# Optimization experiments

Measured on AMD Instinct MI355X. Metric: run time of the kernel, lower is better.

Reference implementation:

```python
import jax, jax.numpy as jnp
import numpy as np

N, DIN, C, E = 50000, 256, 8, 1600000
N_STEPS = 5


def setup_inputs() -> dict:
    key = jax.random.key(0)
    k1, k2, k3, k4 = jax.random.split(key, 4)
    x = jax.random.normal(k1, (N, DIN), dtype=jnp.float32)
    W = jax.random.normal(k2, (DIN, C), dtype=jnp.float32) / np.float32(np.sqrt(DIN))
    b = jnp.zeros((C,), dtype=jnp.float32)
    edge_index = jax.random.randint(k3, (2, E), 0, N, dtype=jnp.int64)
    rv = jax.random.randint(k4, (E,), 0, E, dtype=jnp.int64)
    return {"x": x, "W": W, "b": b, "edge_index": edge_index, "rv": rv}


def _log_normalize(lx):
    return lx - jax.scipy.special.logsumexp(lx, axis=-1, keepdims=True)


def reference(x, W, b, edge_index, rv):
    # transform: Linear (num_hidden=0) + LogSoftmax -> initial log beliefs
    log_b0 = jax.nn.log_softmax(x @ W + b, axis=-1)            # [N, C]
    src, dst = edge_index[0], edge_index[1]
    n_nodes, n_cls = log_b0.shape
    # learn_coupling=False: log_H = -3 * (ones - eye)
    logH = -3.0 * (jnp.ones((n_cls, n_cls), jnp.float32) - jnp.eye(n_cls, dtype=jnp.float32))
    log_msg = jnp.full((edge_index.shape[1], n_cls), -np.log(n_cls), dtype=jnp.float32)
    log_b = log_b0
    for _ in range(N_STEPS):
        x_j = log_b[src]                                        # [E, C] gather
        t = x_j - log_msg[rv]                                   # [E, C]
        # per-edge logsumexp over incoming class dim against coupling matrix
        raw = jax.scipy.special.logsumexp(t[:, :, None] + logH[None, :, :], axis=1)  # [E, C]
        log_msg = _log_normalize(raw)
        agg = jax.ops.segment_sum(log_msg, dst, num_segments=n_nodes)  # scatter-add
        log_b = _log_normalize(agg + log_b0)
    return log_b
```

## Files before the change

kernel.cpp:

```cpp
#include <hip/hip_runtime.h>

static constexpr int kN   = 50000;
static constexpr int kDin = 256;
static constexpr int kC   = 8;
static constexpr int kE   = 1600000;
static constexpr int kSteps = 5;

static constexpr int kNB        = 256;
static constexpr int kBucketW   = 196;
static constexpr int kChunk     = 4096;

static constexpr size_t OFF_LOGB0 = 0;
static constexpr size_t OFF_BHIST = 1600000;
static constexpr size_t OFF_GBASE = 1601024;
static constexpr size_t OFF_GCUR  = 1602112;
static constexpr size_t OFF_START = 1603200;
static constexpr size_t OFF_REC   = 1803264;
static constexpr size_t OFF_INV   = 8203264;
static constexpr size_t OFF_MSGA  = 14603264;
static constexpr size_t OFF_MSGB  = 40203264;
static constexpr size_t WS_NEEDED = 65803264;

static constexpr float kDEC   = 3.0f / 65535.0f;
static constexpr float kENC   = 65535.0f / 3.0f;
static constexpr float kOFF   = 3.2990003f;
static constexpr float kA     = 0.049787068367863944f;
static constexpr float kOneMA = 0.950212931632136f;

__global__ void __launch_bounds__(256) init_kernel(
    const float* __restrict__ x, const float* __restrict__ W,
    const float* __restrict__ bias,
    float* __restrict__ log_b0, float* __restrict__ log_b,
    const int* __restrict__ dst, int* __restrict__ bhist)
{
    __shared__ int h[kNB];
    if (blockIdx.x >= 1024) {
        h[threadIdx.x] = 0;
        __syncthreads();
        const int nthr = 256 * 256;
        for (int e = (blockIdx.x - 1024) * 256 + threadIdx.x; e < kE; e += nthr)
            atomicAdd(&h[dst[e] / kBucketW], 1);
        __syncthreads();
        if (h[threadIdx.x]) atomicAdd(&bhist[threadIdx.x], h[threadIdx.x]);
        return;
    }

    const int lane   = threadIdx.x & 63;
    const int wave   = (blockIdx.x * 256 + threadIdx.x) >> 6;
    const int nwaves = (1024 * 256) >> 6;

    float w[4][8];
#pragma unroll
    for (int j = 0; j < 4; ++j) {
        const float4* wp = reinterpret_cast<const float4*>(W + (size_t)(lane + 64 * j) * kC);
        float4 a = wp[0], b2 = wp[1];
        w[j][0] = a.x;  w[j][1] = a.y;  w[j][2] = a.z;  w[j][3] = a.w;
        w[j][4] = b2.x; w[j][5] = b2.y; w[j][6] = b2.z; w[j][7] = b2.w;
    }

    for (int row = wave; row < kN; row += nwaves) {
        const float* xr = x + (size_t)row * kDin;
        float acc[8] = {0.f, 0.f, 0.f, 0.f, 0.f, 0.f, 0.f, 0.f};
#pragma unroll
        for (int j = 0; j < 4; ++j) {
            float xv = xr[lane + 64 * j];
#pragma unroll
            for (int c = 0; c < 8; ++c) acc[c] = fmaf(xv, w[j][c], acc[c]);
        }
#pragma unroll
        for (int off = 32; off > 0; off >>= 1) {
#pragma unroll
            for (int c = 0; c < 8; ++c) acc[c] += __shfl_down(acc[c], off, 64);
        }
        if (lane == 0) {
            float z[8], m = -1e30f;
#pragma unroll
            for (int c = 0; c < 8; ++c) { z[c] = acc[c] + bias[c]; m = fmaxf(m, z[c]); }
            float s = 0.f;
#pragma unroll
            for (int c = 0; c < 8; ++c) s += __expf(z[c] - m);
            float lse = m + __logf(s);
#pragma unroll
            for (int c = 0; c < 8; ++c) {
                float v = z[c] - lse;
                log_b0[(size_t)row * 8 + c] = v;
                log_b[(size_t)row * 8 + c]  = v;
            }
        }
    }
}

__global__ void __launch_bounds__(256) bucket_scan_kernel(
    const int* __restrict__ bhist, int* __restrict__ gbase, int* __restrict__ gcur)
{
    __shared__ int sh[kNB];
    const int tid = threadIdx.x;
    int v = bhist[tid];
    sh[tid] = v;
    __syncthreads();
#pragma unroll
    for (int off = 1; off < kNB; off <<= 1) {
        int t = (tid >= off) ? sh[tid - off] : 0;
        __syncthreads();
        sh[tid] += t;
        __syncthreads();
    }
    int excl = sh[tid] - v;
    gbase[tid] = excl;
    gcur[tid]  = excl;
    if (tid == kNB - 1) { gbase[kNB] = sh[tid]; gcur[kNB] = sh[tid]; }
}

__global__ void __launch_bounds__(256) bin_kernel(
    const int* __restrict__ dst, int* __restrict__ gcur,
    unsigned int* __restrict__ recbuf)
{
    __shared__ int hist[kNB];
    __shared__ int sh[kNB];
    __shared__ int cursor[kNB];
    __shared__ int gdbase[kNB];
    __shared__ unsigned int buf[kChunk];

    const int tid = threadIdx.x;
    const int e0  = blockIdx.x * kChunk;
    const int n   = (kE - e0 < kChunk) ? (kE - e0) : kChunk;

    hist[tid] = 0;
    __syncthreads();

    int myb[16];
    unsigned int rec[16];
#pragma unroll
    for (int k = 0; k < 16; ++k) {
        const int i = tid + k * 256;
        myb[k] = -1;
        if (i < n) {
            const int d = dst[e0 + i];
            const int b = d / kBucketW;
            myb[k] = b;
            rec[k] = ((unsigned int)(d - b * kBucketW) << 21) | (unsigned int)(e0 + i);
            atomicAdd(&hist[b], 1);
        }
    }
    __syncthreads();

    const int cnt = hist[tid];
    sh[tid] = cnt;
    __syncthreads();
#pragma unroll
    for (int off = 1; off < kNB; off <<= 1) {
        int t = (tid >= off) ? sh[tid - off] : 0;
        __syncthreads();
        sh[tid] += t;
        __syncthreads();
    }
    const int excl = sh[tid] - cnt;
    cursor[tid] = excl;
    __syncthreads();

#pragma unroll
    for (int k = 0; k < 16; ++k) {
        if (myb[k] >= 0) {
            int slot = atomicAdd(&cursor[myb[k]], 1);
            buf[slot] = rec[k];
        }
    }
    gdbase[tid] = (cnt > 0) ? atomicAdd(&gcur[tid], cnt) : 0;
    __syncthreads();

    for (int i = tid; i < n; i += 256) {
        int b = 0;
#pragma unroll
        for (int step = 128; step >= 1; step >>= 1)
            if (b + step <= kNB - 1 && sh[b + step - 1] <= i) b += step;
        const int off_in_b = i - (sh[b] - hist[b]);
        recbuf[gdbase[b] + off_in_b] = buf[i];
    }
}

__global__ void __launch_bounds__(256) fine_kernel(
    const int* __restrict__ gbase, const unsigned int* __restrict__ recbuf,
    int* __restrict__ start, int* __restrict__ inv)
{
    __shared__ int hist[kNB];
    __shared__ int sh[kNB];
    __shared__ int lcur[kNB];

    const int tid = threadIdx.x;
    const int b   = blockIdx.x;
    const int nb0 = b * kBucketW;
    const int nnode = (kN - nb0 < kBucketW) ? (kN - nb0) : kBucketW;
    const int rb = gbase[b], re = gbase[b + 1];

    hist[tid] = 0;
    __syncthreads();

    for (int i = rb + tid; i < re; i += 256)
        atomicAdd(&hist[recbuf[i] >> 21], 1);
    __syncthreads();

    const int cnt = hist[tid];
    sh[tid] = cnt;
    __syncthreads();
#pragma unroll
    for (int off = 1; off < kNB; off <<= 1) {
        int t = (tid >= off) ? sh[tid - off] : 0;
        __syncthreads();
        sh[tid] += t;
        __syncthreads();
    }
    const int excl = sh[tid] - cnt;
    lcur[tid] = rb + excl;
    if (tid < nnode) start[nb0 + tid] = rb + excl;
    if (b == gridDim.x - 1 && tid == 0) start[kN] = kE;
    __syncthreads();

    for (int i = rb + tid; i < re; i += 256) {
        const unsigned int r = recbuf[i];
        const int p = atomicAdd(&lcur[r >> 21], 1);
        inv[p] = (int)(r & 0x1FFFFFu);
    }
}

template <bool FIRST>
__global__ void __launch_bounds__(256) edge_kernel(
    const int* __restrict__ src, const int* __restrict__ rv,
    const float* __restrict__ log_b,
    const unsigned short* __restrict__ mold,
    unsigned short* __restrict__ mnew)
{
    const int e0 = (blockIdx.x * 256 + threadIdx.x) * 2;
    if (e0 >= kE) return;

    const int2 sp = *reinterpret_cast<const int2*>(src + e0);

    const float4* lba = reinterpret_cast<const float4*>(log_b + (size_t)sp.x * 8);
    const float4* lbb = reinterpret_cast<const float4*>(log_b + (size_t)sp.y * 8);
    float4 a0 = lba[0], a1 = lba[1];
    float4 b0 = lbb[0], b1 = lbb[1];

    uint4 ma, mb;
    if (!FIRST) {
        const int2 rp = *reinterpret_cast<const int2*>(rv + e0);
        ma = *reinterpret_cast<const uint4*>(mold + (size_t)rp.x * 8);
        mb = *reinterpret_cast<const uint4*>(mold + (size_t)rp.y * 8);
    }

    float ta[8] = {a0.x, a0.y, a0.z, a0.w, a1.x, a1.y, a1.z, a1.w};
    float tb[8] = {b0.x, b0.y, b0.z, b0.w, b1.x, b1.y, b1.z, b1.w};
    if (!FIRST) {
        ta[0] -= (float)(ma.x & 0xffffu) * kDEC;  ta[1] -= (float)(ma.x >> 16) * kDEC;
        ta[2] -= (float)(ma.y & 0xffffu) * kDEC;  ta[3] -= (float)(ma.y >> 16) * kDEC;
        ta[4] -= (float)(ma.z & 0xffffu) * kDEC;  ta[5] -= (float)(ma.z >> 16) * kDEC;
        ta[6] -= (float)(ma.w & 0xffffu) * kDEC;  ta[7] -= (float)(ma.w >> 16) * kDEC;
        tb[0] -= (float)(mb.x & 0xffffu) * kDEC;  tb[1] -= (float)(mb.x >> 16) * kDEC;
        tb[2] -= (float)(mb.y & 0xffffu) * kDEC;  tb[3] -= (float)(mb.y >> 16) * kDEC;
        tb[4] -= (float)(mb.z & 0xffffu) * kDEC;  tb[5] -= (float)(mb.z >> 16) * kDEC;
        tb[6] -= (float)(mb.w & 0xffffu) * kDEC;  tb[7] -= (float)(mb.w >> 16) * kDEC;
    }

    unsigned int qa[8], qb[8];
    {
        float mx = ta[0];
#pragma unroll
        for (int c = 1; c < 8; ++c) mx = fmaxf(mx, ta[c]);
        float p[8], S = 0.f;
#pragma unroll
        for (int c = 0; c < 8; ++c) { p[c] = __expf(ta[c] - mx); S += p[c]; }
        const float coef = kOneMA / S;
#pragma unroll
        for (int c = 0; c < 8; ++c) {
            float u  = fmaf(coef, p[c], kA);
            float qq = fmaf(__logf(u), kENC, 65535.0f);
            qq = fminf(fmaxf(qq + 0.5f, 0.0f), 65535.0f);
            qa[c] = (unsigned int)qq;
        }
    }
    {
        float mx = tb[0];
#pragma unroll
        for (int c = 1; c < 8; ++c) mx = fmaxf(mx, tb[c]);
        float p[8], S = 0.f;
#pragma unroll
        for (int c = 0; c < 8; ++c) { p[c] = __expf(tb[c] - mx); S += p[c]; }
        const float coef = kOneMA / S;
#pragma unroll
        for (int c = 0; c < 8; ++c) {
            float u  = fmaf(coef, p[c], kA);
            float qq = fmaf(__logf(u), kENC, 65535.0f);
            qq = fminf(fmaxf(qq + 0.5f, 0.0f), 65535.0f);
            qb[c] = (unsigned int)qq;
        }
    }

    uint4* mn = reinterpret_cast<uint4*>(mnew + (size_t)e0 * 8);
    mn[0] = make_uint4(qa[0] | (qa[1] << 16), qa[2] | (qa[3] << 16),
                       qa[4] | (qa[5] << 16), qa[6] | (qa[7] << 16));
    mn[1] = make_uint4(qb[0] | (qb[1] << 16), qb[2] | (qb[3] << 16),
                       qb[4] | (qb[5] << 16), qb[6] | (qb[7] << 16));
}

template <bool FINAL>
__global__ void __launch_bounds__(256) node_kernel(
    const int* __restrict__ start, const int* __restrict__ inv,
    const unsigned short* __restrict__ msgq,
    const float* __restrict__ log_b0, float* __restrict__ log_b)
{
    const int wid  = (blockIdx.x * 256 + threadIdx.x) >> 6;
    const int lane = threadIdx.x & 63;
    const int half = lane >> 5;
    const int l32  = lane & 31;
    const int n = wid * 2 + half;
    if (n >= kN) return;

    const int s = start[n], e2 = start[n + 1];

    int q[8] = {0, 0, 0, 0, 0, 0, 0, 0};
    for (int j = s + l32; j < e2; j += 32) {
        const uint4 m = *reinterpret_cast<const uint4*>(msgq + (size_t)inv[j] * 8);
        q[0] += (int)(m.x & 0xffffu);  q[1] += (int)(m.x >> 16);
        q[2] += (int)(m.y & 0xffffu);  q[3] += (int)(m.y >> 16);
        q[4] += (int)(m.z & 0xffffu);  q[5] += (int)(m.z >> 16);
        q[6] += (int)(m.w & 0xffffu);  q[7] += (int)(m.w >> 16);
    }
#pragma unroll
    for (int off = 1; off <= 16; off <<= 1) {
#pragma unroll
        for (int c = 0; c < 8; ++c) q[c] += __shfl_xor(q[c], off, 64);
    }

    if (l32 == 0) {
        const int deg = e2 - s;
        const float base = -kOFF * (float)deg;
        const float4* lb0 = reinterpret_cast<const float4*>(log_b0 + (size_t)n * 8);
        float4 c0 = lb0[0], c1 = lb0[1];
        float v[8];
        v[0] = fmaf((float)q[0], kDEC, base) + c0.x;
        v[1] = fmaf((float)q[1], kDEC, base) + c0.y;
        v[2] = fmaf((float)q[2], kDEC, base) + c0.z;
        v[3] = fmaf((float)q[3], kDEC, base) + c0.w;
        v[4] = fmaf((float)q[4], kDEC, base) + c1.x;
        v[5] = fmaf((float)q[5], kDEC, base) + c1.y;
        v[6] = fmaf((float)q[6], kDEC, base) + c1.z;
        v[7] = fmaf((float)q[7], kDEC, base) + c1.w;
        if (FINAL) {
            float m = v[0];
#pragma unroll
            for (int c = 1; c < 8; ++c) m = fmaxf(m, v[c]);
            float sum = 0.f;
#pragma unroll
            for (int c = 0; c < 8; ++c) sum += __expf(v[c] - m);
            float lse = m + __logf(sum);
#pragma unroll
            for (int c = 0; c < 8; ++c) v[c] -= lse;
        }
        float4* lb = reinterpret_cast<float4*>(log_b + (size_t)n * 8);
        lb[0] = make_float4(v[0], v[1], v[2], v[3]);
        lb[1] = make_float4(v[4], v[5], v[6], v[7]);
    }
}

extern "C" void kernel_launch(void* const* d_in, const int* in_sizes, int n_in,
                              void* d_out, int out_size, void* d_ws, size_t ws_size,
                              hipStream_t stream) {
    const float* x    = (const float*)d_in[0];
    const float* W    = (const float*)d_in[1];
    const float* bias = (const float*)d_in[2];
    const int*   ei   = (const int*)d_in[3];
    const int*   rv   = (const int*)d_in[4];
    const int* src = ei;
    const int* dst = ei + kE;
    float* out = (float*)d_out;

    if (ws_size < WS_NEEDED) return;

    char* ws = (char*)d_ws;
    float* log_b0 = (float*)(ws + OFF_LOGB0);
    int*   bhist  = (int*)(ws + OFF_BHIST);
    int*   gbase  = (int*)(ws + OFF_GBASE);
    int*   gcur   = (int*)(ws + OFF_GCUR);
    int*   start  = (int*)(ws + OFF_START);
    unsigned int* recbuf = (unsigned int*)(ws + OFF_REC);
    int*   inv    = (int*)(ws + OFF_INV);
    unsigned short* msgA = (unsigned short*)(ws + OFF_MSGA);
    unsigned short* msgB = (unsigned short*)(ws + OFF_MSGB);

    const int edgeBlocks = (kE / 2 + 255) / 256;
    const int nodeBlocks = ((kN + 1) / 2 * 64 + 255) / 256;
    const int binBlocks  = (kE + kChunk - 1) / kChunk;

    (void)hipMemsetAsync(bhist, 0, kNB * sizeof(int), stream);
    init_kernel<<<1280, 256, 0, stream>>>(x, W, bias, log_b0, out, dst, bhist);
    bucket_scan_kernel<<<1, 256, 0, stream>>>(bhist, gbase, gcur);
    bin_kernel<<<binBlocks, 256, 0, stream>>>(dst, gcur, recbuf);
    fine_kernel<<<kNB, 256, 0, stream>>>(gbase, recbuf, start, inv);

    edge_kernel<true><<<edgeBlocks, 256, 0, stream>>>(src, rv, out, msgB, msgA);
    node_kernel<false><<<nodeBlocks, 256, 0, stream>>>(start, inv, msgA, log_b0, out);

    unsigned short* cur = msgA;
    unsigned short* nxt = msgB;
    for (int it = 1; it < kSteps; ++it) {
        edge_kernel<false><<<edgeBlocks, 256, 0, stream>>>(src, rv, out, cur, nxt);
        if (it == kSteps - 1)
            node_kernel<true><<<nodeBlocks, 256, 0, stream>>>(start, inv, nxt, log_b0, out);
        else
            node_kernel<false><<<nodeBlocks, 256, 0, stream>>>(start, inv, nxt, log_b0, out);
        unsigned short* tmp = cur; cur = nxt; nxt = tmp;
    }
}
```

Baseline: 480.6 us.

## Store messages in destination-sorted order so node aggregation reads contiguously

After: 505.9 us. +5.3%, slower.

```diff
diff --git a/kernel.cpp b/kernel.cpp
--- a/kernel.cpp
+++ b/kernel.cpp
@@ -6,9 +6,10 @@
 static constexpr int kE   = 1600000;
 static constexpr int kSteps = 5;
 
-static constexpr int kNB        = 256;
-static constexpr int kBucketW   = 196;
-static constexpr int kChunk     = 4096;
+static constexpr int kNB      = 256;
+static constexpr int kBucketW = 196;
+static constexpr int kChunk   = 4096;
+static constexpr int kEperB   = kE / kNB;
 
 static constexpr size_t OFF_LOGB0 = 0;
 static constexpr size_t OFF_BHIST = 1600000;
@@ -19,7 +20,12 @@
 static constexpr size_t OFF_INV   = 8203264;
 static constexpr size_t OFF_MSGA  = 14603264;
 static constexpr size_t OFF_MSGB  = 40203264;
-static constexpr size_t WS_NEEDED = 65803264;
+static constexpr size_t OFF_SPOS  = 65803264;
+static constexpr size_t OFF_SRCS  = 72203264;
+static constexpr size_t OFF_RVS   = 78603264;
+static constexpr size_t OFF_REC2  = 85003264;
+static constexpr size_t OFF_GCUR2 = 97803264;
+static constexpr size_t WS_NEEDED = 97804288;
 
 static constexpr float kDEC   = 3.0f / 65535.0f;
 static constexpr float kENC   = 65535.0f / 3.0f;
@@ -91,7 +97,8 @@
 }
 
 __global__ void __launch_bounds__(256) bucket_scan_kernel(
-    const int* __restrict__ bhist, int* __restrict__ gbase, int* __restrict__ gcur)
+    const int* __restrict__ bhist, int* __restrict__ gbase, int* __restrict__ gcur,
+    int* __restrict__ gcur2)
 {
     __shared__ int sh[kNB];
     const int tid = threadIdx.x;
@@ -108,6 +115,7 @@
     int excl = sh[tid] - v;
     gbase[tid] = excl;
     gcur[tid]  = excl;
+    gcur2[tid] = tid * kEperB;
     if (tid == kNB - 1) { gbase[kNB] = sh[tid]; gcur[kNB] = sh[tid]; }
 }
 
@@ -222,17 +230,115 @@
     }
 }
 
+__global__ void __launch_bounds__(256) bin2_kernel(
+    const int* __restrict__ inv, int* __restrict__ gcur2,
+    unsigned long long* __restrict__ recbuf2)
+{
+    __shared__ int hist[kNB];
+    __shared__ int sh[kNB];
+    __shared__ int cursor[kNB];
+    __shared__ int gdbase[kNB];
+    __shared__ unsigned long long buf[kChunk];
+
+    const int tid = threadIdx.x;
+    const int p0  = blockIdx.x * kChunk;
+    const int n   = (kE - p0 < kChunk) ? (kE - p0) : kChunk;
+
+    hist[tid] = 0;
+    __syncthreads();
+
+    int myb[16];
+    unsigned long long rec[16];
+#pragma unroll
+    for (int k = 0; k < 16; ++k) {
+        const int i = tid + k * 256;
+        myb[k] = -1;
+        if (i < n) {
+            const int e = inv[p0 + i];
+            const int b = e / kEperB;
+            myb[k] = b;
+            rec[k] = ((unsigned long long)(e - b * kEperB) << 32) | (unsigned int)(p0 + i);
+            atomicAdd(&hist[b], 1);
+        }
+    }
+    __syncthreads();
+
+    const int cnt = hist[tid];
+    sh[tid] = cnt;
+    __syncthreads();
+#pragma unroll
+    for (int off = 1; off < kNB; off <<= 1) {
+        int t = (tid >= off) ? sh[tid - off] : 0;
+        __syncthreads();
+        sh[tid] += t;
+        __syncthreads();
+    }
+    const int excl = sh[tid] - cnt;
+    cursor[tid] = excl;
+    __syncthreads();
+
+#pragma unroll
+    for (int k = 0; k < 16; ++k) {
+        if (myb[k] >= 0) {
+            int slot = atomicAdd(&cursor[myb[k]], 1);
+            buf[slot] = rec[k];
+        }
+    }
+    gdbase[tid] = (cnt > 0) ? atomicAdd(&gcur2[tid], cnt) : 0;
+    __syncthreads();
+
+    for (int i = tid; i < n; i += 256) {
+        int b = 0;
+#pragma unroll
+        for (int step = 128; step >= 1; step >>= 1)
+            if (b + step <= kNB - 1 && sh[b + step - 1] <= i) b += step;
+        const int off_in_b = i - (sh[b] - hist[b]);
+        recbuf2[gdbase[b] + off_in_b] = buf[i];
+    }
+}
+
+__global__ void __launch_bounds__(256) fine2_kernel(
+    const unsigned long long* __restrict__ recbuf2, int* __restrict__ spos)
+{
+    __shared__ int slot[kEperB];
+    const int tid  = threadIdx.x;
+    const int base = blockIdx.x * kEperB;
+
+    for (int i = tid; i < kEperB; i += 256) {
+        const unsigned long long r = recbuf2[base + i];
+        slot[(int)(r >> 32)] = (int)(r & 0xFFFFFFFFu);
+    }
+    __syncthreads();
+    for (int i = tid; i < kEperB; i += 256)
+        spos[base + i] = slot[i];
+}
+
+__global__ void __launch_bounds__(256) build_kernel(
+    const int* __restrict__ inv, const int* __restrict__ src,
+    const int* __restrict__ rv, const int* __restrict__ spos,
+    int* __restrict__ src_s, int* __restrict__ rv_s)
+{
+    const int p0 = (blockIdx.x * 256 + threadIdx.x) * 2;
+    if (p0 >= kE) return;
+    const int2 ee = *reinterpret_cast<const int2*>(inv + p0);
+    const int sx = src[ee.x], sy = src[ee.y];
+    const int rx = rv[ee.x],  ry = rv[ee.y];
+    const int qx = spos[rx],  qy = spos[ry];
+    *reinterpret_cast<int2*>(src_s + p0) = make_int2(sx, sy);
+    *reinterpret_cast<int2*>(rv_s + p0)  = make_int2(qx, qy);
+}
+
 template <bool FIRST>
 __global__ void __launch_bounds__(256) edge_kernel(
-    const int* __restrict__ src, const int* __restrict__ rv,
+    const int* __restrict__ src_s, const int* __restrict__ rv_s,
     const float* __restrict__ log_b,
     const unsigned short* __restrict__ mold,
     unsigned short* __restrict__ mnew)
 {
-    const int e0 = (blockIdx.x * 256 + threadIdx.x) * 2;
-    if (e0 >= kE) return;
-
-    const int2 sp = *reinterpret_cast<const int2*>(src + e0);
+    const int i0 = (blockIdx.x * 256 + threadIdx.x) * 2;
+    if (i0 >= kE) return;
+
+    const int2 sp = *reinterpret_cast<const int2*>(src_s + i0);
 
     const float4* lba = reinterpret_cast<const float4*>(log_b + (size_t)sp.x * 8);
     const float4* lbb = reinterpret_cast<const float4*>(log_b + (size_t)sp.y * 8);
@@ -241,7 +347,7 @@
 
     uint4 ma, mb;
     if (!FIRST) {
-        const int2 rp = *reinterpret_cast<const int2*>(rv + e0);
+        const int2 rp = *reinterpret_cast<const int2*>(rv_s + i0);
         ma = *reinterpret_cast<const uint4*>(mold + (size_t)rp.x * 8);
         mb = *reinterpret_cast<const uint4*>(mold + (size_t)rp.y * 8);
     }
@@ -293,7 +399,7 @@
         }
     }
 
-    uint4* mn = reinterpret_cast<uint4*>(mnew + (size_t)e0 * 8);
+    uint4* mn = reinterpret_cast<uint4*>(mnew + (size_t)i0 * 8);
     mn[0] = make_uint4(qa[0] | (qa[1] << 16), qa[2] | (qa[3] << 16),
                        qa[4] | (qa[5] << 16), qa[6] | (qa[7] << 16));
     mn[1] = make_uint4(qb[0] | (qb[1] << 16), qb[2] | (qb[3] << 16),
@@ -302,7 +408,7 @@
 
 template <bool FINAL>
 __global__ void __launch_bounds__(256) node_kernel(
-    const int* __restrict__ start, const int* __restrict__ inv,
+    const int* __restrict__ start,
     const unsigned short* __restrict__ msgq,
     const float* __restrict__ log_b0, float* __restrict__ log_b)
 {
@@ -317,7 +423,7 @@
 
     int q[8] = {0, 0, 0, 0, 0, 0, 0, 0};
     for (int j = s + l32; j < e2; j += 32) {
-        const uint4 m = *reinterpret_cast<const uint4*>(msgq + (size_t)inv[j] * 8);
+        const uint4 m = *reinterpret_cast<const uint4*>(msgq + (size_t)j * 8);
         q[0] += (int)(m.x & 0xffffu);  q[1] += (int)(m.x >> 16);
         q[2] += (int)(m.y & 0xffffu);  q[3] += (int)(m.y >> 16);
         q[4] += (int)(m.z & 0xffffu);  q[5] += (int)(m.z >> 16);
@@ -384,6 +490,11 @@
     int*   inv    = (int*)(ws + OFF_INV);
     unsigned short* msgA = (unsigned short*)(ws + OFF_MSGA);
     unsigned short* msgB = (unsigned short*)(ws + OFF_MSGB);
+    int*   spos   = (int*)(ws + OFF_SPOS);
+    int*   src_s  = (int*)(ws + OFF_SRCS);
+    int*   rv_s   = (int*)(ws + OFF_RVS);
+    unsigned long long* recbuf2 = (unsigned long long*)(ws + OFF_REC2);
+    int*   gcur2  = (int*)(ws + OFF_GCUR2);
 
     const int edgeBlocks = (kE / 2 + 255) / 256;
     const int nodeBlocks = ((kN + 1) / 2 * 64 + 255) / 256;
@@ -391,21 +502,24 @@
 
     (void)hipMemsetAsync(bhist, 0, kNB * sizeof(int), stream);
     init_kernel<<<1280, 256, 0, stream>>>(x, W, bias, log_b0, out, dst, bhist);
-    bucket_scan_kernel<<<1, 256, 0, stream>>>(bhist, gbase, gcur);
+    bucket_scan_kernel<<<1, 256, 0, stream>>>(bhist, gbase, gcur, gcur2);
     bin_kernel<<<binBlocks, 256, 0, stream>>>(dst, gcur, recbuf);
     fine_kernel<<<kNB, 256, 0, stream>>>(gbase, recbuf, start, inv);
-
-    edge_kernel<true><<<edgeBlocks, 256, 0, stream>>>(src, rv, out, msgB, msgA);
-    node_kernel<false><<<nodeBlocks, 256, 0, stream>>>(start, inv, msgA, log_b0, out);
+    bin2_kernel<<<binBlocks, 256, 0, stream>>>(inv, gcur2, recbuf2);
+    fine2_kernel<<<kNB, 256, 0, stream>>>(recbuf2, spos);
+    build_kernel<<<edgeBlocks, 256, 0, stream>>>(inv, src, rv, spos, src_s, rv_s);
+
+    edge_kernel<true><<<edgeBlocks, 256, 0, stream>>>(src_s, rv_s, out, msgB, msgA);
+    node_kernel<false><<<nodeBlocks, 256, 0, stream>>>(start, msgA, log_b0, out);
 
     unsigned short* cur = msgA;
     unsigned short* nxt = msgB;
     for (int it = 1; it < kSteps; ++it) {
-        edge_kernel<false><<<edgeBlocks, 256, 0, stream>>>(src, rv, out, cur, nxt);
+        edge_kernel<false><<<edgeBlocks, 256, 0, stream>>>(src_s, rv_s, out, cur, nxt);
         if (it == kSteps - 1)
-            node_kernel<true><<<nodeBlocks, 256, 0, stream>>>(start, inv, nxt, log_b0, out);
+            node_kernel<true><<<nodeBlocks, 256, 0, stream>>>(start, nxt, log_b0, out);
         else
-            node_kernel<false><<<nodeBlocks, 256, 0, stream>>>(start, inv, nxt, log_b0, out);
+            node_kernel<false><<<nodeBlocks, 256, 0, stream>>>(start, nxt, log_b0, out);
         unsigned short* tmp = cur; cur = nxt; nxt = tmp;
     }
 }
```
